# Performance work log

Measured on AMD Instinct MI355X. Metric: run time of the kernel, lower is better.

Reference implementation:

```python
import jax, jax.numpy as jnp
import numpy as np

SEQ_LEN, BATCH, VOCAB = 128, 32, 32000
EMB, HID = 32, 16


def setup_inputs() -> dict:
    key = jax.random.key(0)
    ks = jax.random.split(key, 10)
    return {
        "input_batch": jax.random.randint(ks[0], (SEQ_LEN, BATCH), 0, VOCAB, dtype=jnp.int64)
        if jax.config.jax_enable_x64 else jax.random.randint(ks[0], (SEQ_LEN, BATCH), 0, VOCAB, dtype=jnp.int32),
        "h0_lr": jax.random.uniform(ks[1], (BATCH, HID), dtype=jnp.float32),
        "h0_rl": jax.random.uniform(ks[2], (BATCH, HID), dtype=jnp.float32),
        "embedding": jax.random.normal(ks[3], (VOCAB, EMB), dtype=jnp.float32),
        "W_lr": jax.random.normal(ks[4], (HID, EMB + HID), dtype=jnp.float32) * 0.25,
        "b_lr": jax.random.normal(ks[5], (HID,), dtype=jnp.float32) * 0.25,
        "W_rl": jax.random.normal(ks[6], (HID, EMB + HID), dtype=jnp.float32) * 0.25,
        "b_rl": jax.random.normal(ks[7], (HID,), dtype=jnp.float32) * 0.25,
        "W_ho": jax.random.normal(ks[8], (VOCAB, 2 * HID), dtype=jnp.float32) * 0.25,
        "b_ho": jax.random.normal(ks[9], (VOCAB,), dtype=jnp.float32) * 0.25,
    }


def _rnn_step(W, b):
    # h_{t+1} = tanh([x_t, h_t] @ W^T + b)
    def f(h, x):
        h_new = jnp.tanh(jnp.concatenate([x, h], axis=-1) @ W.T + b)
        return h_new, h_new
    return f


def reference(input_batch, h0_lr, h0_rl, embedding, W_lr, b_lr, W_rl, b_rl, W_ho, b_ho):
    emb = embedding[input_batch]  # [S, B, EMB]
    # Left-to-right: consumes emb[0..S-2]; hLR[0] = h0_lr, len S
    _, hs_lr = jax.lax.scan(_rnn_step(W_lr, b_lr), h0_lr, emb[:-1])
    hLR = jnp.concatenate([h0_lr[None], hs_lr], axis=0)  # [S, B, HID]
    # Right-to-left: consumes emb[S-1 .. 1]; hRL[0] = h0_rl, len S
    _, hs_rl = jax.lax.scan(_rnn_step(W_rl, b_rl), h0_rl, emb[:0:-1])
    hRL = jnp.concatenate([h0_rl[None], hs_rl], axis=0)  # [S, B, HID]
    # prediction[i] pairs hLR[i] with hRL[S-1-i]
    combined = jnp.concatenate([hLR, hRL[::-1]], axis=-1)  # [S, B, 2*HID]
    logits = combined @ W_ho.T + b_ho  # [S, B, VOCAB]
    return jax.nn.log_softmax(logits, axis=-1)
```

## Files before the change

### kernel.cpp

```cpp
#include <hip/hip_runtime.h>
#include <hip/hip_bf16.h>
#include <math.h>

#define SS 128
#define BB 32
#define VV 32000
#define EE 32
#define HH 16
#define KK 32
#define NROWS (SS*BB)
#define NSL 16
#define VT 125
#define NPRE 8
#define WSL 40
#define WVT 50

typedef __attribute__((ext_vector_type(4))) float f32x4;
typedef __attribute__((ext_vector_type(8))) short bf16x8;
typedef __attribute__((ext_vector_type(4))) short s16x4;

#define DPPF(x, ctrl) __builtin_bit_cast(float, __builtin_amdgcn_update_dpp( \
    __builtin_bit_cast(int, (x)), __builtin_bit_cast(int, (x)), (ctrl), 0xF, 0xF, false))

__global__ __launch_bounds__(256) void k_prep(
    const float* __restrict__ Who, __hip_bfloat16* __restrict__ who_bf,
    const int* __restrict__ tok, const float* __restrict__ emb,
    const float* __restrict__ Wlr, const float* __restrict__ blr,
    const float* __restrict__ Wrl, const float* __restrict__ brl,
    float* __restrict__ xp) {
  if (blockIdx.x < 1000) {
    int i = blockIdx.x * 256 + threadIdx.x;
    f32x4 v = ((const f32x4*)Who)[i];
    s16x4 o;
    #pragma unroll
    for (int q = 0; q < 4; ++q) {
      __hip_bfloat16 h = __float2bfloat16(v[q]);
      o[q] = *reinterpret_cast<short*>(&h);
    }
    ((s16x4*)who_bf)[i] = o;
  } else {
    int g = (blockIdx.x - 1000) * 256 + threadIdx.x;
    int dir = g >> 16;
    int rem = g & 65535;
    int t = rem >> 9;
    int b = (rem >> 4) & 31;
    int j = rem & 15;
    const float* W  = dir ? Wrl : Wlr;
    const float* bv = dir ? brl : blr;
    int tk = tok[t*BB + b];
    const float* er = emb + tk*EE;
    const float* wr = W + j*(EE+HH);
    float acc = bv[j];
    #pragma unroll
    for (int k = 0; k < EE; ++k) acc += er[k] * wr[k];
    xp[g] = acc;
  }
}

__global__ __launch_bounds__(128) void k_rnn_fused(
    const float* __restrict__ xp,
    const float* __restrict__ h0lr, const float* __restrict__ h0rl,
    const float* __restrict__ Wlr, const float* __restrict__ Wrl,
    __hip_bfloat16* __restrict__ comb_bf) {
  int bid = blockIdx.x;
  int dir = bid >> 2;
  int b = (bid & 3) * 8 + (threadIdx.x >> 4);
  int j = threadIdx.x & 15;
  const float* W  = dir ? Wrl : Wlr;
  const float* h0 = dir ? h0rl : h0lr;
  float wr[HH];
  #pragma unroll
  for (int r = 0; r < HH; ++r) wr[r] = W[j*(EE+HH) + EE + (j ^ r)];
  const float* x = xp + dir * (SS*BB*HH);
  int u = b*HH + j;
  float h = h0[u];
  if (dir == 0) comb_bf[0*(BB*KK) + b*KK + j] = __float2bfloat16(h);
  else          comb_bf[(SS-1)*(BB*KK) + b*KK + HH + j] = __float2bfloat16(h);
  float xbuf[NPRE];
  #pragma unroll
  for (int p = 0; p < NPRE; ++p) {
    int tt = 1 + p;
    int off = dir ? (SS-tt)*(BB*HH) + u : (tt-1)*(BB*HH) + u;
    xbuf[p] = x[off];
  }
  for (int tc = 1; tc < SS; tc += NPRE) {
    #pragma unroll
    for (int i = 0; i < NPRE; ++i) {
      int t = tc + i;
      if (t < SS) {
        float xv = xbuf[i];
        int tp = t + NPRE;
        int offp = (tp < SS) ? (dir ? (SS-tp)*(BB*HH) + u : (tp-1)*(BB*HH) + u) : u;
        xbuf[i] = x[offp];
        float t1  = DPPF(h, 0xB1);
        float t2  = DPPF(h, 0x4E);
        float t3  = DPPF(h, 0x1B);
        float t7  = DPPF(h, 0x141);
        float t15 = DPPF(h, 0x140);
        float t4  = DPPF(t7, 0x1B);
        float t5  = DPPF(t7, 0x4E);
        float t6  = DPPF(t7, 0xB1);
        float t8  = DPPF(t15, 0x141);
        float t12 = DPPF(t15, 0x1B);
        float t13 = DPPF(t15, 0x4E);
        float t14 = DPPF(t15, 0xB1);
        float t9  = DPPF(t8, 0xB1);
        float t10 = DPPF(t8, 0x4E);
        float t11 = DPPF(t8, 0x1B);
        float a0 = fmaf(wr[0], h,  xv);
        a0 = fmaf(wr[4],  t4,  a0);
        a0 = fmaf(wr[8],  t8,  a0);
        a0 = fmaf(wr[12], t12, a0);
        float a1 = wr[1] * t1;
        a1 = fmaf(wr[5],  t5,  a1);
        a1 = fmaf(wr[9],  t9,  a1);
        a1 = fmaf(wr[13], t13, a1);
        float a2 = wr[2] * t2;
        a2 = fmaf(wr[6],  t6,  a2);
        a2 = fmaf(wr[10], t10, a2);
        a2 = fmaf(wr[14], t14, a2);
        float a3 = wr[3] * t3;
        a3 = fmaf(wr[7],  t7,  a3);
        a3 = fmaf(wr[11], t11, a3);
        a3 = fmaf(wr[15], t15, a3);
        float acc = (a0 + a1) + (a2 + a3);
        float e = __expf(2.f * acc);
        h = fmaf(-2.f, __builtin_amdgcn_rcpf(e + 1.f), 1.f);
        int ci = dir ? ((SS-1-t)*(BB*KK) + b*KK + HH + j)
                     : (t*(BB*KK) + b*KK + j);
        comb_bf[ci] = __float2bfloat16(h);
      }
    }
  }
}

__global__ __launch_bounds__(256) void k_sumexp(
    const __hip_bfloat16* __restrict__ cb, const __hip_bfloat16* __restrict__ wb,
    const float* __restrict__ bho, float* __restrict__ part) {
  int wg = ((blockIdx.x & 7) << 7) | (blockIdx.x >> 3);
  int w = wg * 4 + (threadIdx.x >> 6);
  int lane = threadIdx.x & 63;
  int rt = w >> 4;
  int sl = w & 15;
  int v0 = sl * (VT*16);
  int g = lane >> 4, c = lane & 15;
  bf16x8 bfr = *(const bf16x8*)(cb + (size_t)(rt*16 + c)*KK + g*8);
  float s = 0.f;
  for (int t = 0; t < VT; ++t) {
    int v = v0 + t*16;
    bf16x8 af = *(const bf16x8*)(wb + (size_t)(v + c)*KK + g*8);
    f32x4 bh = *(const f32x4*)(bho + v + g*4);
    f32x4 d = __builtin_amdgcn_mfma_f32_16x16x32_bf16(af, bfr, bh, 0, 0, 0);
    s += __expf(d[0]) + __expf(d[1]) + __expf(d[2]) + __expf(d[3]);
  }
  s += __shfl_xor(s, 16);
  s += __shfl_xor(s, 32);
  if (lane < 16)
    part[(size_t)(rt*16 + lane)*NSL + sl] = s;
}

__global__ __launch_bounds__(256) void k_write(
    const __hip_bfloat16* __restrict__ cb, const __hip_bfloat16* __restrict__ wb,
    const float* __restrict__ bho, const float* __restrict__ part,
    float* __restrict__ out) {
  __shared__ char afl[WVT * 1024];
  __shared__ float bhl[WVT * 16];
  int bid = blockIdx.x;
  int wg = ((bid & 7) * 320) + (bid >> 3);
  int rtg = wg / WSL;
  int sl  = wg % WSL;
  int v0  = sl * (WVT*16);
  int tid = threadIdx.x;
  const f32x4* src = (const f32x4*)(wb + (size_t)v0 * KK);
  for (int o = tid; o < WVT*64; o += 256) {
    f32x4 v = src[o];
    int t = o >> 6, u = o & 63;
    int us = u ^ ((u >> 3) & 7);
    *(f32x4*)(afl + t*1024 + us*16) = v;
  }
  for (int o = tid; o < WVT*16; o += 256) bhl[o] = bho[v0 + o];
  __syncthreads();
  int wid = tid >> 6, lane = tid & 63;
  int rt = rtg*4 + wid;
  int g = lane >> 4, c = lane & 15;
  size_t row = (size_t)rt*16 + c;
  const f32x4* pp = (const f32x4*)(part + row*NSL);
  f32x4 p0 = pp[0], p1 = pp[1], p2 = pp[2], p3 = pp[3];
  float s = (p0[0]+p0[1]+p0[2]+p0[3]) + (p1[0]+p1[1]+p1[2]+p1[3])
          + (p2[0]+p2[1]+p2[2]+p2[3]) + (p3[0]+p3[1]+p3[2]+p3[3]);
  float Lr = logf(s);
  bf16x8 bfr = *(const bf16x8*)(cb + row*KK + g*8);
  int u = c*4 + g;
  int us = u ^ ((u >> 3) & 7);
  const char* afp = afl + us*16;
  float* op = out + row*VV + v0 + g*4;
  for (int t = 0; t < WVT; ++t) {
    bf16x8 a = *(const bf16x8*)(afp + t*1024);
    f32x4 bh = *(const f32x4*)(bhl + t*16 + g*4);
    f32x4 cin = bh - Lr;
    f32x4 d = __builtin_amdgcn_mfma_f32_16x16x32_bf16(a, bfr, cin, 0, 0, 0);
    *(f32x4*)(op + t*16) = d;
  }
}

extern "C" void kernel_launch(void* const* d_in, const int* in_sizes, int n_in,
                              void* d_out, int out_size, void* d_ws, size_t ws_size,
                              hipStream_t stream) {
  const int*   tok  = (const int*)d_in[0];
  const float* h0lr = (const float*)d_in[1];
  const float* h0rl = (const float*)d_in[2];
  const float* emb  = (const float*)d_in[3];
  const float* Wlr  = (const float*)d_in[4];
  const float* blr  = (const float*)d_in[5];
  const float* Wrl  = (const float*)d_in[6];
  const float* brl  = (const float*)d_in[7];
  const float* Who  = (const float*)d_in[8];
  const float* bho  = (const float*)d_in[9];
  float* out = (float*)d_out;
  float* ws  = (float*)d_ws;

  float* xp   = ws;
  float* part = ws + 131072;
  __hip_bfloat16* comb_bf = (__hip_bfloat16*)(ws + 196608);
  __hip_bfloat16* who_bf  = (__hip_bfloat16*)(ws + 262144);

  hipLaunchKernelGGL(k_prep, dim3(1512), dim3(256), 0, stream,
                     Who, who_bf, tok, emb, Wlr, blr, Wrl, brl, xp);
  hipLaunchKernelGGL(k_rnn_fused, dim3(8), dim3(128), 0, stream,
                     xp, h0lr, h0rl, Wlr, Wrl, comb_bf);
  hipLaunchKernelGGL(k_sumexp, dim3(1024), dim3(256), 0, stream,
                     comb_bf, who_bf, bho, part);
  hipLaunchKernelGGL(k_write, dim3(2560), dim3(256), 0, stream,
                     comb_bf, who_bf, bho, part, out);
}
```

Before: 192.6 us.

## Fuse all four stages into one cooperative persistent kernel with grid syncs

Replaces the four separate kernel launches with a single cooperative kernel of 512 blocks that runs prep, the RNN recurrence, the sum-exp pass and the output write, separated by grid-wide barriers. The goal is to remove launch gaps and inter-kernel drain/fill. While four blocks run the serial RNN, the other blocks read the bf16 weight matrix to warm the cache. The cost is that the RNN phase now runs with fewer, larger blocks (16 batches per block), and the later phases are looped over a fixed grid, where grid.sync overhead and reduced occupancy could offset the savings.

```diff
diff --git a/kernel.cpp b/kernel.cpp
--- a/kernel.cpp
+++ b/kernel.cpp
@@ -1,6 +1,9 @@
 #include <hip/hip_runtime.h>
 #include <hip/hip_bf16.h>
+#include <hip/hip_cooperative_groups.h>
 #include <math.h>
+
+namespace cg = cooperative_groups;
 
 #define SS 128
 #define BB 32
@@ -22,24 +25,35 @@
 #define DPPF(x, ctrl) __builtin_bit_cast(float, __builtin_amdgcn_update_dpp( \
     __builtin_bit_cast(int, (x)), __builtin_bit_cast(int, (x)), (ctrl), 0xF, 0xF, false))
 
-__global__ __launch_bounds__(256) void k_prep(
-    const float* __restrict__ Who, __hip_bfloat16* __restrict__ who_bf,
-    const int* __restrict__ tok, const float* __restrict__ emb,
+__global__ __launch_bounds__(256, 2) void k_mega(
+    const int* __restrict__ tok,
+    const float* __restrict__ h0lr, const float* __restrict__ h0rl,
+    const float* __restrict__ emb,
     const float* __restrict__ Wlr, const float* __restrict__ blr,
     const float* __restrict__ Wrl, const float* __restrict__ brl,
-    float* __restrict__ xp) {
-  if (blockIdx.x < 1000) {
-    int i = blockIdx.x * 256 + threadIdx.x;
-    f32x4 v = ((const f32x4*)Who)[i];
-    s16x4 o;
-    #pragma unroll
-    for (int q = 0; q < 4; ++q) {
-      __hip_bfloat16 h = __float2bfloat16(v[q]);
-      o[q] = *reinterpret_cast<short*>(&h);
-    }
-    ((s16x4*)who_bf)[i] = o;
-  } else {
-    int g = (blockIdx.x - 1000) * 256 + threadIdx.x;
+    const float* __restrict__ Who, const float* __restrict__ bho,
+    float* __restrict__ out, float* __restrict__ xp,
+    float* __restrict__ part, __hip_bfloat16* __restrict__ comb_bf,
+    __hip_bfloat16* __restrict__ who_bf) {
+  cg::grid_group grid = cg::this_grid();
+  __shared__ char  afl[WVT * 1024];
+  __shared__ float bhl[WVT * 16];
+  const int bid = blockIdx.x;
+  const int tid = threadIdx.x;
+
+  {
+    for (int o = tid; o < 500; o += 256) {
+      int i = bid * 500 + o;
+      f32x4 v = ((const f32x4*)Who)[i];
+      s16x4 w;
+      #pragma unroll
+      for (int q = 0; q < 4; ++q) {
+        __hip_bfloat16 h = __float2bfloat16(v[q]);
+        w[q] = *reinterpret_cast<short*>(&h);
+      }
+      ((s16x4*)who_bf)[i] = w;
+    }
+    int g = bid * 256 + tid;
     int dir = g >> 16;
     int rem = g & 65535;
     int t = rem >> 9;
@@ -55,151 +69,152 @@
     for (int k = 0; k < EE; ++k) acc += er[k] * wr[k];
     xp[g] = acc;
   }
-}
-
-__global__ __launch_bounds__(128) void k_rnn_fused(
-    const float* __restrict__ xp,
-    const float* __restrict__ h0lr, const float* __restrict__ h0rl,
-    const float* __restrict__ Wlr, const float* __restrict__ Wrl,
-    __hip_bfloat16* __restrict__ comb_bf) {
-  int bid = blockIdx.x;
-  int dir = bid >> 2;
-  int b = (bid & 3) * 8 + (threadIdx.x >> 4);
-  int j = threadIdx.x & 15;
-  const float* W  = dir ? Wrl : Wlr;
-  const float* h0 = dir ? h0rl : h0lr;
-  float wr[HH];
-  #pragma unroll
-  for (int r = 0; r < HH; ++r) wr[r] = W[j*(EE+HH) + EE + (j ^ r)];
-  const float* x = xp + dir * (SS*BB*HH);
-  int u = b*HH + j;
-  float h = h0[u];
-  if (dir == 0) comb_bf[0*(BB*KK) + b*KK + j] = __float2bfloat16(h);
-  else          comb_bf[(SS-1)*(BB*KK) + b*KK + HH + j] = __float2bfloat16(h);
-  float xbuf[NPRE];
-  #pragma unroll
-  for (int p = 0; p < NPRE; ++p) {
-    int tt = 1 + p;
-    int off = dir ? (SS-tt)*(BB*HH) + u : (tt-1)*(BB*HH) + u;
-    xbuf[p] = x[off];
-  }
-  for (int tc = 1; tc < SS; tc += NPRE) {
+  __threadfence();
+  grid.sync();
+
+  if (bid < 4) {
+    int dir = bid >> 1;
+    int b = (bid & 1) * 16 + (tid >> 4);
+    int j = tid & 15;
+    const float* W  = dir ? Wrl : Wlr;
+    const float* h0 = dir ? h0rl : h0lr;
+    float wr[HH];
     #pragma unroll
-    for (int i = 0; i < NPRE; ++i) {
-      int t = tc + i;
-      if (t < SS) {
-        float xv = xbuf[i];
-        int tp = t + NPRE;
-        int offp = (tp < SS) ? (dir ? (SS-tp)*(BB*HH) + u : (tp-1)*(BB*HH) + u) : u;
-        xbuf[i] = x[offp];
-        float t1  = DPPF(h, 0xB1);
-        float t2  = DPPF(h, 0x4E);
-        float t3  = DPPF(h, 0x1B);
-        float t7  = DPPF(h, 0x141);
-        float t15 = DPPF(h, 0x140);
-        float t4  = DPPF(t7, 0x1B);
-        float t5  = DPPF(t7, 0x4E);
-        float t6  = DPPF(t7, 0xB1);
-        float t8  = DPPF(t15, 0x141);
-        float t12 = DPPF(t15, 0x1B);
-        float t13 = DPPF(t15, 0x4E);
-        float t14 = DPPF(t15, 0xB1);
-        float t9  = DPPF(t8, 0xB1);
-        float t10 = DPPF(t8, 0x4E);
-        float t11 = DPPF(t8, 0x1B);
-        float a0 = fmaf(wr[0], h,  xv);
-        a0 = fmaf(wr[4],  t4,  a0);
-        a0 = fmaf(wr[8],  t8,  a0);
-        a0 = fmaf(wr[12], t12, a0);
-        float a1 = wr[1] * t1;
-        a1 = fmaf(wr[5],  t5,  a1);
-        a1 = fmaf(wr[9],  t9,  a1);
-        a1 = fmaf(wr[13], t13, a1);
-        float a2 = wr[2] * t2;
-        a2 = fmaf(wr[6],  t6,  a2);
-        a2 = fmaf(wr[10], t10, a2);
-        a2 = fmaf(wr[14], t14, a2);
-        float a3 = wr[3] * t3;
-        a3 = fmaf(wr[7],  t7,  a3);
-        a3 = fmaf(wr[11], t11, a3);
-        a3 = fmaf(wr[15], t15, a3);
-        float acc = (a0 + a1) + (a2 + a3);
-        float e = __expf(2.f * acc);
-        h = fmaf(-2.f, __builtin_amdgcn_rcpf(e + 1.f), 1.f);
-        int ci = dir ? ((SS-1-t)*(BB*KK) + b*KK + HH + j)
-                     : (t*(BB*KK) + b*KK + j);
-        comb_bf[ci] = __float2bfloat16(h);
+    for (int r = 0; r < HH; ++r) wr[r] = W[j*(EE+HH) + EE + (j ^ r)];
+    const float* x = xp + dir * (SS*BB*HH);
+    int u = b*HH + j;
+    float h = h0[u];
+    if (dir == 0) comb_bf[0*(BB*KK) + b*KK + j] = __float2bfloat16(h);
+    else          comb_bf[(SS-1)*(BB*KK) + b*KK + HH + j] = __float2bfloat16(h);
+    float xbuf[NPRE];
+    #pragma unroll
+    for (int p = 0; p < NPRE; ++p) {
+      int tt = 1 + p;
+      int off = dir ? (SS-tt)*(BB*HH) + u : (tt-1)*(BB*HH) + u;
+      xbuf[p] = x[off];
+    }
+    for (int tc = 1; tc < SS; tc += NPRE) {
+      #pragma unroll
+      for (int i = 0; i < NPRE; ++i) {
+        int t = tc + i;
+        if (t < SS) {
+          float xv = xbuf[i];
+          int tp = t + NPRE;
+          int offp = (tp < SS) ? (dir ? (SS-tp)*(BB*HH) + u : (tp-1)*(BB*HH) + u) : u;
+          xbuf[i] = x[offp];
+          float t1  = DPPF(h, 0xB1);
+          float t2  = DPPF(h, 0x4E);
+          float t3  = DPPF(h, 0x1B);
+          float t7  = DPPF(h, 0x141);
+          float t15 = DPPF(h, 0x140);
+          float t4  = DPPF(t7, 0x1B);
+          float t5  = DPPF(t7, 0x4E);
+          float t6  = DPPF(t7, 0xB1);
+          float t8  = DPPF(t15, 0x141);
+          float t12 = DPPF(t15, 0x1B);
+          float t13 = DPPF(t15, 0x4E);
+          float t14 = DPPF(t15, 0xB1);
+          float t9  = DPPF(t8, 0xB1);
+          float t10 = DPPF(t8, 0x4E);
+          float t11 = DPPF(t8, 0x1B);
+          float a0 = fmaf(wr[0], h,  xv);
+          a0 = fmaf(wr[4],  t4,  a0);
+          a0 = fmaf(wr[8],  t8,  a0);
+          a0 = fmaf(wr[12], t12, a0);
+          float a1 = wr[1] * t1;
+          a1 = fmaf(wr[5],  t5,  a1);
+          a1 = fmaf(wr[9],  t9,  a1);
+          a1 = fmaf(wr[13], t13, a1);
+          float a2 = wr[2] * t2;
+          a2 = fmaf(wr[6],  t6,  a2);
+          a2 = fmaf(wr[10], t10, a2);
+          a2 = fmaf(wr[14], t14, a2);
+          float a3 = wr[3] * t3;
+          a3 = fmaf(wr[7],  t7,  a3);
+          a3 = fmaf(wr[11], t11, a3);
+          a3 = fmaf(wr[15], t15, a3);
+          float acc = (a0 + a1) + (a2 + a3);
+          float e = __expf(2.f * acc);
+          h = fmaf(-2.f, __builtin_amdgcn_rcpf(e + 1.f), 1.f);
+          int ci = dir ? ((SS-1-t)*(BB*KK) + b*KK + HH + j)
+                       : (t*(BB*KK) + b*KK + j);
+          comb_bf[ci] = __float2bfloat16(h);
+        }
       }
     }
-  }
-}
-
-__global__ __launch_bounds__(256) void k_sumexp(
-    const __hip_bfloat16* __restrict__ cb, const __hip_bfloat16* __restrict__ wb,
-    const float* __restrict__ bho, float* __restrict__ part) {
-  int wg = ((blockIdx.x & 7) << 7) | (blockIdx.x >> 3);
-  int w = wg * 4 + (threadIdx.x >> 6);
-  int lane = threadIdx.x & 63;
-  int rt = w >> 4;
-  int sl = w & 15;
-  int v0 = sl * (VT*16);
-  int g = lane >> 4, c = lane & 15;
-  bf16x8 bfr = *(const bf16x8*)(cb + (size_t)(rt*16 + c)*KK + g*8);
-  float s = 0.f;
-  for (int t = 0; t < VT; ++t) {
-    int v = v0 + t*16;
-    bf16x8 af = *(const bf16x8*)(wb + (size_t)(v + c)*KK + g*8);
-    f32x4 bh = *(const f32x4*)(bho + v + g*4);
-    f32x4 d = __builtin_amdgcn_mfma_f32_16x16x32_bf16(af, bfr, bh, 0, 0, 0);
-    s += __expf(d[0]) + __expf(d[1]) + __expf(d[2]) + __expf(d[3]);
-  }
-  s += __shfl_xor(s, 16);
-  s += __shfl_xor(s, 32);
-  if (lane < 16)
-    part[(size_t)(rt*16 + lane)*NSL + sl] = s;
-}
-
-__global__ __launch_bounds__(256) void k_write(
-    const __hip_bfloat16* __restrict__ cb, const __hip_bfloat16* __restrict__ wb,
-    const float* __restrict__ bho, const float* __restrict__ part,
-    float* __restrict__ out) {
-  __shared__ char afl[WVT * 1024];
-  __shared__ float bhl[WVT * 16];
-  int bid = blockIdx.x;
-  int wg = ((bid & 7) * 320) + (bid >> 3);
-  int rtg = wg / WSL;
-  int sl  = wg % WSL;
-  int v0  = sl * (WVT*16);
-  int tid = threadIdx.x;
-  const f32x4* src = (const f32x4*)(wb + (size_t)v0 * KK);
-  for (int o = tid; o < WVT*64; o += 256) {
-    f32x4 v = src[o];
-    int t = o >> 6, u = o & 63;
+  } else {
+    const f32x4* wp = (const f32x4*)who_bf;
+    float acc = 0.f;
+    for (int o = (bid - 4) * 256 + tid; o < 128000; o += 508 * 256)
+      acc += wp[o][0];
+    asm volatile("" :: "v"(acc));
+  }
+  __threadfence();
+  grid.sync();
+
+  for (int r = 0; r < 2; ++r) {
+    int uu = r * 512 + bid;
+    int wg = ((uu & 7) << 7) | (uu >> 3);
+    int w = wg * 4 + (tid >> 6);
+    int lane = tid & 63;
+    int rt = w >> 4;
+    int sl = w & 15;
+    int v0 = sl * (VT*16);
+    int g = lane >> 4, c = lane & 15;
+    bf16x8 bfr = *(const bf16x8*)(comb_bf + (size_t)(rt*16 + c)*KK + g*8);
+    float s = 0.f;
+    for (int t = 0; t < VT; ++t) {
+      int v = v0 + t*16;
+      bf16x8 af = *(const bf16x8*)(who_bf + (size_t)(v + c)*KK + g*8);
+      f32x4 bh = *(const f32x4*)(bho + v + g*4);
+      f32x4 d = __builtin_amdgcn_mfma_f32_16x16x32_bf16(af, bfr, bh, 0, 0, 0);
+      s += __expf(d[0]) + __expf(d[1]) + __expf(d[2]) + __expf(d[3]);
+    }
+    s += __shfl_xor(s, 16);
+    s += __shfl_xor(s, 32);
+    if (lane < 16)
+      part[(size_t)(rt*16 + lane)*NSL + sl] = s;
+  }
+  __threadfence();
+  grid.sync();
+
+  for (int r = 0; r < 5; ++r) {
+    int uu = r * 512 + bid;
+    int wg = (uu & 7) * 320 + (uu >> 3);
+    int rtg = wg / WSL;
+    int sl  = wg % WSL;
+    int v0  = sl * (WVT*16);
+    __syncthreads();
+    const f32x4* src = (const f32x4*)(who_bf + (size_t)v0 * KK);
+    for (int o = tid; o < WVT*64; o += 256) {
+      f32x4 v = src[o];
+      int t = o >> 6, u = o & 63;
+      int us = u ^ ((u >> 3) & 7);
+      *(f32x4*)(afl + t*1024 + us*16) = v;
+    }
+    for (int o = tid; o < WVT*16; o += 256) bhl[o] = bho[v0 + o];
+    __syncthreads();
+    int wid = tid >> 6, lane = tid & 63;
+    int rt = rtg*4 + wid;
+    int g = lane >> 4, c = lane & 15;
+    size_t row = (size_t)rt*16 + c;
+    const f32x4* pp = (const f32x4*)(part + row*NSL);
+    f32x4 p0 = pp[0], p1 = pp[1], p2 = pp[2], p3 = pp[3];
+    float s = (p0[0]+p0[1]+p0[2]+p0[3]) + (p1[0]+p1[1]+p1[2]+p1[3])
+            + (p2[0]+p2[1]+p2[2]+p2[3]) + (p3[0]+p3[1]+p3[2]+p3[3]);
+    float Lr = logf(s);
+    bf16x8 bfr = *(const bf16x8*)(comb_bf + row*KK + g*8);
+    int u = c*4 + g;
     int us = u ^ ((u >> 3) & 7);
-    *(f32x4*)(afl + t*1024 + us*16) = v;
-  }
-  for (int o = tid; o < WVT*16; o += 256) bhl[o] = bho[v0 + o];
-  __syncthreads();
-  int wid = tid >> 6, lane = tid & 63;
-  int rt = rtg*4 + wid;
-  int g = lane >> 4, c = lane & 15;
-  size_t row = (size_t)rt*16 + c;
-  const f32x4* pp = (const f32x4*)(part + row*NSL);
-  f32x4 p0 = pp[0], p1 = pp[1], p2 = pp[2], p3 = pp[3];
-  float s = (p0[0]+p0[1]+p0[2]+p0[3]) + (p1[0]+p1[1]+p1[2]+p1[3])
-          + (p2[0]+p2[1]+p2[2]+p2[3]) + (p3[0]+p3[1]+p3[2]+p3[3]);
-  float Lr = logf(s);
-  bf16x8 bfr = *(const bf16x8*)(cb + row*KK + g*8);
-  int u = c*4 + g;
-  int us = u ^ ((u >> 3) & 7);
-  const char* afp = afl + us*16;
-  float* op = out + row*VV + v0 + g*4;
-  for (int t = 0; t < WVT; ++t) {
-    bf16x8 a = *(const bf16x8*)(afp + t*1024);
-    f32x4 bh = *(const f32x4*)(bhl + t*16 + g*4);
-    f32x4 cin = bh - Lr;
-    f32x4 d = __builtin_amdgcn_mfma_f32_16x16x32_bf16(a, bfr, cin, 0, 0, 0);
-    *(f32x4*)(op + t*16) = d;
+    const char* afp = afl + us*16;
+    float* op = out + row*VV + v0 + g*4;
+    for (int t = 0; t < WVT; ++t) {
+      bf16x8 a = *(const bf16x8*)(afp + t*1024);
+      f32x4 bh = *(const f32x4*)(bhl + t*16 + g*4);
+      f32x4 cin = bh - Lr;
+      f32x4 d = __builtin_amdgcn_mfma_f32_16x16x32_bf16(a, bfr, cin, 0, 0, 0);
+      *(f32x4*)(op + t*16) = d;
+    }
   }
 }
 
@@ -224,12 +239,12 @@
   __hip_bfloat16* comb_bf = (__hip_bfloat16*)(ws + 196608);
   __hip_bfloat16* who_bf  = (__hip_bfloat16*)(ws + 262144);
 
-  hipLaunchKernelGGL(k_prep, dim3(1512), dim3(256), 0, stream,
-                     Who, who_bf, tok, emb, Wlr, blr, Wrl, brl, xp);
-  hipLaunchKernelGGL(k_rnn_fused, dim3(8), dim3(128), 0, stream,
-                     xp, h0lr, h0rl, Wlr, Wrl, comb_bf);
-  hipLaunchKernelGGL(k_sumexp, dim3(1024), dim3(256), 0, stream,
-                     comb_bf, who_bf, bho, part);
-  hipLaunchKernelGGL(k_write, dim3(2560), dim3(256), 0, stream,
-                     comb_bf, who_bf, bho, part, out);
+  void* args[] = {
+    (void*)&tok, (void*)&h0lr, (void*)&h0rl, (void*)&emb,
+    (void*)&Wlr, (void*)&blr, (void*)&Wrl, (void*)&brl,
+    (void*)&Who, (void*)&bho,
+    (void*)&out, (void*)&xp, (void*)&part, (void*)&comb_bf, (void*)&who_bf
+  };
+  hipLaunchCooperativeKernel((const void*)k_mega, dim3(512), dim3(256),
+                             args, 0, stream);
 }
```

Result: slower. 433.7 us (+125.2%).
